# Kernel optimization log

Measured on AMD Instinct MI355X. Metric: run time of the kernel, lower is better.

The kernel has to match this reference:

```python
import jax, jax.numpy as jnp
import numpy as np

B, H, SQ, SKV, D = 2, 16, 2048, 2048, 64
SCALE = 8  # sqrt(head_dim)


def setup_inputs() -> dict:
    key = jax.random.key(0)
    kq, kk, kv, km = jax.random.split(key, 4)
    q = jax.random.normal(kq, (B, H, SQ, D), dtype=jnp.float32)
    k = jax.random.normal(kk, (B, H, SKV, D), dtype=jnp.float32)
    v = jax.random.normal(kv, (B, H, SKV, D), dtype=jnp.float32)
    mask = jax.random.normal(km, (1, 1, SQ, SKV), dtype=jnp.float32)
    return {"q": q, "k": k, "v": v, "mask": mask, "scale": SCALE}


def reference(q, k, v, mask, scale):
    # scores: [B, H, SQ, SKV]
    scores = jnp.einsum("bhqd,bhkd->bhqk", q, k) / scale
    scores = scores + mask  # broadcast additive mask
    probs = jax.nn.softmax(scores, axis=-1)
    # hidden: [B, H, SQ, D]
    return jnp.einsum("bhqk,bhkd->bhqd", probs, v)
```

## Files before the change

kernel.cpp:

```cpp
#include <hip/hip_runtime.h>
#include <hip/hip_bf16.h>

#define NB 2
#define NH 16
#define NSQ 2048
#define NSKV 2048
#define ND 64
#define NT (NSKV / 64)
#define LOG2E 1.4426950408889634f
#define BHSTRIDE (NSKV * ND)

typedef __attribute__((ext_vector_type(8))) short bf16x8;
typedef __attribute__((ext_vector_type(4))) float f32x4;

__device__ __forceinline__ short f2bf(float x) {
  union { float f; unsigned u; } c; c.f = x;
  unsigned r = c.u + 0x7fffu + ((c.u >> 16) & 1u);
  return (short)(r >> 16);
}
__device__ __forceinline__ unsigned pack_bf2(float lo, float hi) {
  union { __hip_bfloat162 h; unsigned u; } c;
  c.h = __float22bfloat162_rn(float2{lo, hi});
  return c.u;
}
__device__ __forceinline__ float u2f(unsigned u) {
  union { unsigned u; float f; } c; c.u = u; return c.f;
}
__device__ __forceinline__ float exp2_fast(float x) {
#if __has_builtin(__builtin_amdgcn_exp2f)
  return __builtin_amdgcn_exp2f(x);
#else
  return exp2f(x);
#endif
}

__device__ __forceinline__ int kvmap(int x) {
  return (x & 3) | (((x >> 4) & 1) << 2) | (((x >> 2) & 1) << 3)
       | (((x >> 3) & 1) << 4) | (x & 32);
}

__global__ void prep_k(const float* __restrict__ K, short* __restrict__ Kp) {
  const int bh = blockIdx.y, tile = blockIdx.x, tid = (int)threadIdx.x;
#pragma unroll
  for (int h = 0; h < 2; ++h) {
    const int u    = tid + h * 256;
    const int nt   = u >> 7, kc = (u >> 6) & 1, lane = u & 63;
    const int prow = nt * 16 + (lane & 15);
    const float* src = K + ((size_t)bh * NSKV + tile * 64 + kvmap(prow)) * ND
                         + kc * 32 + (lane >> 4) * 8;
    float4 a = *(const float4*)src, b = *(const float4*)(src + 4);
    bf16x8 w;
    w[0]=f2bf(a.x); w[1]=f2bf(a.y); w[2]=f2bf(a.z); w[3]=f2bf(a.w);
    w[4]=f2bf(b.x); w[5]=f2bf(b.y); w[6]=f2bf(b.z); w[7]=f2bf(b.w);
    *(bf16x8*)(Kp + (size_t)bh * BHSTRIDE + (size_t)tile * 4096 + u * 8) = w;
  }
}

__global__ void prep_vt(const float* __restrict__ V, short* __restrict__ Vp) {
  __shared__ float T[64][65];
  const int kv0 = blockIdx.x * 64;
  const int bh  = blockIdx.y;
  const int t   = (int)threadIdx.x;
  const float* src = V + ((size_t)bh * NSKV + kv0) * ND;
#pragma unroll
  for (int i = 0; i < 4; ++i) {
    float4 v = *(const float4*)(src + (size_t)((t >> 4) + 16 * i) * ND + (t & 15) * 4);
    T[(t >> 4) + 16 * i][(t & 15) * 4 + 0] = v.x;
    T[(t >> 4) + 16 * i][(t & 15) * 4 + 1] = v.y;
    T[(t >> 4) + 16 * i][(t & 15) * 4 + 2] = v.z;
    T[(t >> 4) + 16 * i][(t & 15) * 4 + 3] = v.w;
  }
  __syncthreads();
  const int d = t >> 2, c = t & 3;
  bf16x8 w0, w1;
#pragma unroll
  for (int j = 0; j < 8; ++j) w0[j] = f2bf(T[c * 16 + j][d]);
#pragma unroll
  for (int j = 0; j < 8; ++j) w1[j] = f2bf(T[c * 16 + 8 + j][d]);
  const int frag  = (d >> 4) * 2 + (c >> 1);
  const int lane0 = (((2 * c) & 3) << 4) | (d & 15);
  const int lane1 = (((2 * c + 1) & 3) << 4) | (d & 15);
  short* dstb = Vp + (size_t)bh * BHSTRIDE + (size_t)blockIdx.x * 4096 + frag * 512;
  *(bf16x8*)(dstb + lane0 * 8) = w0;
  *(bf16x8*)(dstb + lane1 * 8) = w1;
}

__global__ void prep_mt(const float* __restrict__ M, unsigned short* __restrict__ Mt) {
  const int qt = blockIdx.x;
  const int kt = blockIdx.y;
  const int t  = (int)threadIdx.x;
  const int rl = t >> 4;
  const int c  = t & 15;
  const int row = qt * 16 + rl;
  float4 v = *(const float4*)(M + (size_t)row * NSKV + kt * 64 + c * 4);
  const int nt   = 2 * (c >> 3) + (c & 1);
  const int lq   = (c >> 1) & 3;
  const int lane = lq * 16 + rl;
  ushort4 o;
  o.x = (unsigned short)f2bf(LOG2E * v.x);
  o.y = (unsigned short)f2bf(LOG2E * v.y);
  o.z = (unsigned short)f2bf(LOG2E * v.z);
  o.w = (unsigned short)f2bf(LOG2E * v.w);
  *(ushort4*)(Mt + (((size_t)qt * 32 + kt) * 64 + lane) * 16 + nt * 4) = o;
}

__global__ __launch_bounds__(256, 2)
void attn_fwd(const float* __restrict__ Q, const short* __restrict__ Kp,
              const short* __restrict__ Vp, const unsigned short* __restrict__ Mt,
              const void* __restrict__ scale_p, float* __restrict__ O)
{
  const int lin = (int)blockIdx.x + ((int)blockIdx.y << 4);
  const int swz = ((lin & 7) << 6) | (lin >> 3);
  const int qb  = swz & 15;
  const int bh  = swz >> 4;

  const int tid = (int)threadIdx.x;
  const int wv  = tid >> 6;
  const int ln  = tid & 63;
  const int l16 = ln & 15;
  const int lq  = ln >> 4;

  float scale_v;
  {
    union { int i; float f; } u;
    u.i = ((const int*)scale_p)[0];
    float af = fabsf(u.f);
    scale_v = (af >= 1e-6f && af <= 1e6f) ? u.f : (float)u.i;
  }
  const float qmul = LOG2E / scale_v;

  const int q0 = qb * 128;
  const short* Kb = Kp + (size_t)bh * BHSTRIDE;
  const short* Vb = Vp + (size_t)bh * BHSTRIDE;

  bf16x8 qf[2][2];
#pragma unroll
  for (int qs = 0; qs < 2; ++qs) {
    const float* qrow = Q + ((size_t)bh * NSQ + q0 + wv * 32 + qs * 16 + l16) * ND;
#pragma unroll
    for (int kc = 0; kc < 2; ++kc) {
      const float4* p = (const float4*)(qrow + kc * 32 + lq * 8);
      float4 a = p[0], b = p[1];
      bf16x8 f;
      f[0]=f2bf(a.x*qmul); f[1]=f2bf(a.y*qmul); f[2]=f2bf(a.z*qmul); f[3]=f2bf(a.w*qmul);
      f[4]=f2bf(b.x*qmul); f[5]=f2bf(b.y*qmul); f[6]=f2bf(b.z*qmul); f[7]=f2bf(b.w*qmul);
      qf[qs][kc] = f;
    }
  }

  f32x4 oa[2][4];
  f32x4 lacc[2];
#pragma unroll
  for (int qs = 0; qs < 2; ++qs) {
#pragma unroll
    for (int dt = 0; dt < 4; ++dt) { f32x4 z = {0.f,0.f,0.f,0.f}; oa[qs][dt] = z; }
    f32x4 z = {0.f,0.f,0.f,0.f}; lacc[qs] = z;
  }

  bf16x8 ones;
#pragma unroll
  for (int j = 0; j < 8; ++j) ones[j] = (short)0x3F80;

  const unsigned short* Mq0 = Mt + ((size_t)(qb * 8 + wv * 2)) * 32 * 64 * 16 + (size_t)ln * 16;
  const unsigned short* Mq1 = Mq0 + (size_t)32 * 64 * 16;

  union MU { uint4 q[2]; unsigned u[8]; };
  MU mc[2], mn[2];

  bf16x8 kfc[4][2], kfn[4][2], vf[4][2];
#pragma unroll
  for (int nt = 0; nt < 4; ++nt)
#pragma unroll
    for (int kc = 0; kc < 2; ++kc)
      kfc[nt][kc] = *(const bf16x8*)(Kb + (nt * 2 + kc) * 512 + ln * 8);
  mc[0].q[0] = *(const uint4*)(Mq0);
  mc[0].q[1] = *(const uint4*)(Mq0 + 8);
  mc[1].q[0] = *(const uint4*)(Mq1);
  mc[1].q[1] = *(const uint4*)(Mq1 + 8);

#pragma unroll 2
  for (int t = 0; t < NT; ++t) {
    const short* Vt0 = Vb + (size_t)t * 4096;
#pragma unroll
    for (int dt = 0; dt < 4; ++dt)
#pragma unroll
      for (int kc = 0; kc < 2; ++kc)
        vf[dt][kc] = *(const bf16x8*)(Vt0 + (dt * 2 + kc) * 512 + ln * 8);

    if (t + 1 < NT) {
      const short* Kt1 = Kb + (size_t)(t + 1) * 4096;
#pragma unroll
      for (int nt = 0; nt < 4; ++nt)
#pragma unroll
        for (int kc = 0; kc < 2; ++kc)
          kfn[nt][kc] = *(const bf16x8*)(Kt1 + (nt * 2 + kc) * 512 + ln * 8);
    }

    f32x4 s0[4];
    __builtin_amdgcn_s_setprio(1);
#pragma unroll
    for (int nt = 0; nt < 4; ++nt) {
      f32x4 a = {0.f,0.f,0.f,0.f};
      a = __builtin_amdgcn_mfma_f32_16x16x32_bf16(kfc[nt][0], qf[0][0], a, 0, 0, 0);
      a = __builtin_amdgcn_mfma_f32_16x16x32_bf16(kfc[nt][1], qf[0][1], a, 0, 0, 0);
      s0[nt] = a;
    }
    __builtin_amdgcn_s_setprio(0);

    bf16x8 pa0[2];
    {
#pragma unroll
      for (int nt = 0; nt < 4; ++nt) {
        const unsigned w0 = mc[0].u[nt * 2], w1 = mc[0].u[nt * 2 + 1];
        s0[nt][0] = exp2_fast(s0[nt][0] + u2f(w0 << 16));
        s0[nt][1] = exp2_fast(s0[nt][1] + u2f(w0 & 0xffff0000u));
        s0[nt][2] = exp2_fast(s0[nt][2] + u2f(w1 << 16));
        s0[nt][3] = exp2_fast(s0[nt][3] + u2f(w1 & 0xffff0000u));
      }
#pragma unroll
      for (int kc = 0; kc < 2; ++kc) {
        union { unsigned u[4]; bf16x8 v; } w;
        w.u[0] = pack_bf2(s0[2*kc][0],   s0[2*kc][1]);
        w.u[1] = pack_bf2(s0[2*kc][2],   s0[2*kc][3]);
        w.u[2] = pack_bf2(s0[2*kc+1][0], s0[2*kc+1][1]);
        w.u[3] = pack_bf2(s0[2*kc+1][2], s0[2*kc+1][3]);
        pa0[kc] = w.v;
      }
    }

    f32x4 s1[4];
    __builtin_amdgcn_s_setprio(1);
#pragma unroll
    for (int nt = 0; nt < 4; ++nt) {
      f32x4 a = {0.f,0.f,0.f,0.f};
      a = __builtin_amdgcn_mfma_f32_16x16x32_bf16(kfc[nt][0], qf[1][0], a, 0, 0, 0);
      a = __builtin_amdgcn_mfma_f32_16x16x32_bf16(kfc[nt][1], qf[1][1], a, 0, 0, 0);
      s1[nt] = a;
    }
    __builtin_amdgcn_s_setprio(0);

    if (t + 1 < NT) {
      const unsigned short* mp0 = Mq0 + (size_t)(t + 1) * 64 * 16;
      const unsigned short* mp1 = Mq1 + (size_t)(t + 1) * 64 * 16;
      mn[0].q[0] = *(const uint4*)(mp0);
      mn[0].q[1] = *(const uint4*)(mp0 + 8);
      mn[1].q[0] = *(const uint4*)(mp1);
      mn[1].q[1] = *(const uint4*)(mp1 + 8);
    }

    __builtin_amdgcn_s_setprio(1);
#pragma unroll
    for (int kc = 0; kc < 2; ++kc) {
#pragma unroll
      for (int dt = 0; dt < 4; ++dt)
        oa[0][dt] = __builtin_amdgcn_mfma_f32_16x16x32_bf16(pa0[kc], vf[dt][kc], oa[0][dt], 0, 0, 0);
      lacc[0] = __builtin_amdgcn_mfma_f32_16x16x32_bf16(pa0[kc], ones, lacc[0], 0, 0, 0);
    }
    __builtin_amdgcn_s_setprio(0);

    bf16x8 pa1[2];
    {
#pragma unroll
      for (int nt = 0; nt < 4; ++nt) {
        const unsigned w0 = mc[1].u[nt * 2], w1 = mc[1].u[nt * 2 + 1];
        s1[nt][0] = exp2_fast(s1[nt][0] + u2f(w0 << 16));
        s1[nt][1] = exp2_fast(s1[nt][1] + u2f(w0 & 0xffff0000u));
        s1[nt][2] = exp2_fast(s1[nt][2] + u2f(w1 << 16));
        s1[nt][3] = exp2_fast(s1[nt][3] + u2f(w1 & 0xffff0000u));
      }
#pragma unroll
      for (int kc = 0; kc < 2; ++kc) {
        union { unsigned u[4]; bf16x8 v; } w;
        w.u[0] = pack_bf2(s1[2*kc][0],   s1[2*kc][1]);
        w.u[1] = pack_bf2(s1[2*kc][2],   s1[2*kc][3]);
        w.u[2] = pack_bf2(s1[2*kc+1][0], s1[2*kc+1][1]);
        w.u[3] = pack_bf2(s1[2*kc+1][2], s1[2*kc+1][3]);
        pa1[kc] = w.v;
      }
    }

    __builtin_amdgcn_s_setprio(1);
#pragma unroll
    for (int kc = 0; kc < 2; ++kc) {
#pragma unroll
      for (int dt = 0; dt < 4; ++dt)
        oa[1][dt] = __builtin_amdgcn_mfma_f32_16x16x32_bf16(pa1[kc], vf[dt][kc], oa[1][dt], 0, 0, 0);
      lacc[1] = __builtin_amdgcn_mfma_f32_16x16x32_bf16(pa1[kc], ones, lacc[1], 0, 0, 0);
    }
    __builtin_amdgcn_s_setprio(0);

#pragma unroll
    for (int nt = 0; nt < 4; ++nt)
#pragma unroll
      for (int kc = 0; kc < 2; ++kc)
        kfc[nt][kc] = kfn[nt][kc];
    mc[0] = mn[0];
    mc[1] = mn[1];
  }

#pragma unroll
  for (int qs = 0; qs < 2; ++qs)
#pragma unroll
    for (int r = 0; r < 4; ++r) {
      const float inv = 1.0f / lacc[qs][r];
      float* orow = O + ((size_t)bh * NSQ + q0 + wv * 32 + qs * 16 + lq * 4 + r) * ND;
#pragma unroll
      for (int dt = 0; dt < 4; ++dt)
        orow[dt * 16 + l16] = oa[qs][dt][r] * inv;
    }
}

extern "C" void kernel_launch(void* const* d_in, const int* in_sizes, int n_in,
                              void* d_out, int out_size, void* d_ws, size_t ws_size,
                              hipStream_t stream) {
  const float* q     = (const float*)d_in[0];
  const float* k     = (const float*)d_in[1];
  const float* v     = (const float*)d_in[2];
  const float* mask  = (const float*)d_in[3];
  const void*  scale = (const void*)d_in[4];
  float* out = (float*)d_out;

  const size_t NELEM = (size_t)NB * NH * NSKV * ND;
  short* Kpk = (short*)d_ws;
  short* Vpk = Kpk + NELEM;
  unsigned short* Mtl = (unsigned short*)(Vpk + NELEM);

  prep_k<<<dim3(NSKV / 64, NB * NH), 256, 0, stream>>>(k, Kpk);
  prep_vt<<<dim3(NSKV / 64, NB * NH), 256, 0, stream>>>(v, Vpk);
  prep_mt<<<dim3(NSQ / 16, NSKV / 64), 256, 0, stream>>>(mask, Mtl);

  dim3 grid(NSQ / 128, NB * NH);
  attn_fwd<<<grid, 256, 0, stream>>>(q, Kpk, Vpk, Mtl, scale, out);
}
```

Measured before the change: 78.87 us.

## Stage K/V tiles through LDS via async loads and fold mask into MFMA accumulator

Replaces per-wave direct global register loads of K and V with a double-buffered LDS stage filled by global_load_lds. Each wave now loads one quarter of the tile and the tile is shared across the block through a barrier. The mask is fed in as the initial MFMA accumulator instead of being added before exp2, and it is kept in fp32 when the workspace is large enough. This cuts redundant global and L2 traffic for K/V and removes the per-element mask adds. In exchange it adds a __syncthreads per tile, uses more LDS, and doubles the mask bytes read in the fp32 path.

```diff
diff --git a/kernel.cpp b/kernel.cpp
--- a/kernel.cpp
+++ b/kernel.cpp
@@ -12,6 +12,8 @@
 
 typedef __attribute__((ext_vector_type(8))) short bf16x8;
 typedef __attribute__((ext_vector_type(4))) float f32x4;
+typedef __attribute__((address_space(1))) const unsigned gas_u32;
+typedef __attribute__((address_space(3))) unsigned las_u32;
 
 __device__ __forceinline__ short f2bf(float x) {
   union { float f; unsigned u; } c; c.f = x;
@@ -85,12 +87,21 @@
   *(bf16x8*)(dstb + lane1 * 8) = w1;
 }
 
+__global__ void prep_mf(const float* __restrict__ M, float* __restrict__ Mf) {
+  const int qt = blockIdx.x, kt = blockIdx.y, t = (int)threadIdx.x;
+  const int rl = t >> 4, c = t & 15;
+  const int row = qt * 16 + rl;
+  float4 v = *(const float4*)(M + (size_t)row * NSKV + kt * 64 + c * 4);
+  const int nt   = 2 * (c >> 3) + (c & 1);
+  const int lq   = (c >> 1) & 3;
+  const int lane = lq * 16 + rl;
+  float4 o = {LOG2E * v.x, LOG2E * v.y, LOG2E * v.z, LOG2E * v.w};
+  *(float4*)(Mf + (((size_t)qt * 32 + kt) * 64 + lane) * 16 + nt * 4) = o;
+}
+
 __global__ void prep_mt(const float* __restrict__ M, unsigned short* __restrict__ Mt) {
-  const int qt = blockIdx.x;
-  const int kt = blockIdx.y;
-  const int t  = (int)threadIdx.x;
-  const int rl = t >> 4;
-  const int c  = t & 15;
+  const int qt = blockIdx.x, kt = blockIdx.y, t = (int)threadIdx.x;
+  const int rl = t >> 4, c = t & 15;
   const int row = qt * 16 + rl;
   float4 v = *(const float4*)(M + (size_t)row * NSKV + kt * 64 + c * 4);
   const int nt   = 2 * (c >> 3) + (c & 1);
@@ -104,9 +115,10 @@
   *(ushort4*)(Mt + (((size_t)qt * 32 + kt) * 64 + lane) * 16 + nt * 4) = o;
 }
 
+template<bool MF32>
 __global__ __launch_bounds__(256, 2)
 void attn_fwd(const float* __restrict__ Q, const short* __restrict__ Kp,
-              const short* __restrict__ Vp, const unsigned short* __restrict__ Mt,
+              const short* __restrict__ Vp, const void* __restrict__ Mv,
               const void* __restrict__ scale_p, float* __restrict__ O)
 {
   const int lin = (int)blockIdx.x + ((int)blockIdx.y << 4);
@@ -132,6 +144,9 @@
   const int q0 = qb * 128;
   const short* Kb = Kp + (size_t)bh * BHSTRIDE;
   const short* Vb = Vp + (size_t)bh * BHSTRIDE;
+
+  __shared__ short Kl[2][4096];
+  __shared__ short Vl[2][4096];
 
   bf16x8 qf[2][2];
 #pragma unroll
@@ -161,141 +176,115 @@
 #pragma unroll
   for (int j = 0; j < 8; ++j) ones[j] = (short)0x3F80;
 
-  const unsigned short* Mq0 = Mt + ((size_t)(qb * 8 + wv * 2)) * 32 * 64 * 16 + (size_t)ln * 16;
-  const unsigned short* Mq1 = Mq0 + (size_t)32 * 64 * 16;
-
-  union MU { uint4 q[2]; unsigned u[8]; };
-  MU mc[2], mn[2];
-
-  bf16x8 kfc[4][2], kfn[4][2], vf[4][2];
-#pragma unroll
-  for (int nt = 0; nt < 4; ++nt)
-#pragma unroll
-    for (int kc = 0; kc < 2; ++kc)
-      kfc[nt][kc] = *(const bf16x8*)(Kb + (nt * 2 + kc) * 512 + ln * 8);
-  mc[0].q[0] = *(const uint4*)(Mq0);
-  mc[0].q[1] = *(const uint4*)(Mq0 + 8);
-  mc[1].q[0] = *(const uint4*)(Mq1);
-  mc[1].q[1] = *(const uint4*)(Mq1 + 8);
-
-#pragma unroll 2
-  for (int t = 0; t < NT; ++t) {
-    const short* Vt0 = Vb + (size_t)t * 4096;
-#pragma unroll
-    for (int dt = 0; dt < 4; ++dt)
-#pragma unroll
-      for (int kc = 0; kc < 2; ++kc)
-        vf[dt][kc] = *(const bf16x8*)(Vt0 + (dt * 2 + kc) * 512 + ln * 8);
-
+  const int ebytes = MF32 ? 4 : 2;
+  const char* M0 = (const char*)Mv + ((size_t)(qb * 8 + wv * 2) * 32768 + (size_t)ln * 16) * ebytes;
+  const char* M1 = M0 + (size_t)32768 * ebytes;
+
+  auto mload = [&](int t, float4* mf0, float4* mf1) {
+    if constexpr (MF32) {
+      const float* p0 = (const float*)(M0 + (size_t)t * 1024 * 4);
+      const float* p1 = (const float*)(M1 + (size_t)t * 1024 * 4);
+#pragma unroll
+      for (int nt = 0; nt < 4; ++nt) {
+        mf0[nt] = *(const float4*)(p0 + nt * 4);
+        mf1[nt] = *(const float4*)(p1 + nt * 4);
+      }
+    } else {
+      const unsigned short* p0 = (const unsigned short*)(M0 + (size_t)t * 1024 * 2);
+      const unsigned short* p1 = (const unsigned short*)(M1 + (size_t)t * 1024 * 2);
+      uint4 a0 = *(const uint4*)p0, b0 = *(const uint4*)(p0 + 8);
+      uint4 a1 = *(const uint4*)p1, b1 = *(const uint4*)(p1 + 8);
+      const unsigned u0[8] = {a0.x,a0.y,a0.z,a0.w,b0.x,b0.y,b0.z,b0.w};
+      const unsigned u1[8] = {a1.x,a1.y,a1.z,a1.w,b1.x,b1.y,b1.z,b1.w};
+#pragma unroll
+      for (int nt = 0; nt < 4; ++nt) {
+        mf0[nt] = float4{u2f(u0[nt*2] << 16), u2f(u0[nt*2] & 0xffff0000u),
+                         u2f(u0[nt*2+1] << 16), u2f(u0[nt*2+1] & 0xffff0000u)};
+        mf1[nt] = float4{u2f(u1[nt*2] << 16), u2f(u1[nt*2] & 0xffff0000u),
+                         u2f(u1[nt*2+1] << 16), u2f(u1[nt*2+1] & 0xffff0000u)};
+      }
+    }
+  };
+
+  auto stage = [&](int t, int buf) {
+    const short* ks = Kb + (size_t)t * 4096;
+    const short* vs = Vb + (size_t)t * 4096;
+#pragma unroll
+    for (int i = 0; i < 2; ++i) {
+      const int chunk = wv * 2 + i;
+      __builtin_amdgcn_global_load_lds((gas_u32*)(ks + chunk * 512 + ln * 8),
+                                       (las_u32*)&Kl[buf][chunk * 512], 16, 0, 0);
+      __builtin_amdgcn_global_load_lds((gas_u32*)(vs + chunk * 512 + ln * 8),
+                                       (las_u32*)&Vl[buf][chunk * 512], 16, 0, 0);
+    }
+  };
+
+  auto subtile = [&](bf16x8 (&kf)[4][2], bf16x8 (&vf)[4][2], int qs, float4* mf) {
+    f32x4 s[4];
+    __builtin_amdgcn_s_setprio(1);
+#pragma unroll
+    for (int nt = 0; nt < 4; ++nt) {
+      f32x4 a = *(const f32x4*)&mf[nt];
+      a = __builtin_amdgcn_mfma_f32_16x16x32_bf16(kf[nt][0], qf[qs][0], a, 0, 0, 0);
+      a = __builtin_amdgcn_mfma_f32_16x16x32_bf16(kf[nt][1], qf[qs][1], a, 0, 0, 0);
+      s[nt] = a;
+    }
+    __builtin_amdgcn_s_setprio(0);
+#pragma unroll
+    for (int nt = 0; nt < 4; ++nt) {
+      s[nt][0] = exp2_fast(s[nt][0]);
+      s[nt][1] = exp2_fast(s[nt][1]);
+      s[nt][2] = exp2_fast(s[nt][2]);
+      s[nt][3] = exp2_fast(s[nt][3]);
+    }
+    bf16x8 pa[2];
+#pragma unroll
+    for (int kc = 0; kc < 2; ++kc) {
+      union { unsigned u[4]; bf16x8 v; } w;
+      w.u[0] = pack_bf2(s[2*kc][0],   s[2*kc][1]);
+      w.u[1] = pack_bf2(s[2*kc][2],   s[2*kc][3]);
+      w.u[2] = pack_bf2(s[2*kc+1][0], s[2*kc+1][1]);
+      w.u[3] = pack_bf2(s[2*kc+1][2], s[2*kc+1][3]);
+      pa[kc] = w.v;
+    }
+    __builtin_amdgcn_s_setprio(1);
+#pragma unroll
+    for (int kc = 0; kc < 2; ++kc) {
+#pragma unroll
+      for (int dt = 0; dt < 4; ++dt)
+        oa[qs][dt] = __builtin_amdgcn_mfma_f32_16x16x32_bf16(pa[kc], vf[dt][kc], oa[qs][dt], 0, 0, 0);
+      lacc[qs] = __builtin_amdgcn_mfma_f32_16x16x32_bf16(pa[kc], ones, lacc[qs], 0, 0, 0);
+    }
+    __builtin_amdgcn_s_setprio(0);
+  };
+
+  auto tile = [&](int t, int buf, float4 (&mc0)[4], float4 (&mc1)[4],
+                  float4 (&mn0)[4], float4 (&mn1)[4]) {
     if (t + 1 < NT) {
-      const short* Kt1 = Kb + (size_t)(t + 1) * 4096;
-#pragma unroll
-      for (int nt = 0; nt < 4; ++nt)
-#pragma unroll
-        for (int kc = 0; kc < 2; ++kc)
-          kfn[nt][kc] = *(const bf16x8*)(Kt1 + (nt * 2 + kc) * 512 + ln * 8);
-    }
-
-    f32x4 s0[4];
-    __builtin_amdgcn_s_setprio(1);
-#pragma unroll
-    for (int nt = 0; nt < 4; ++nt) {
-      f32x4 a = {0.f,0.f,0.f,0.f};
-      a = __builtin_amdgcn_mfma_f32_16x16x32_bf16(kfc[nt][0], qf[0][0], a, 0, 0, 0);
-      a = __builtin_amdgcn_mfma_f32_16x16x32_bf16(kfc[nt][1], qf[0][1], a, 0, 0, 0);
-      s0[nt] = a;
-    }
-    __builtin_amdgcn_s_setprio(0);
-
-    bf16x8 pa0[2];
-    {
-#pragma unroll
-      for (int nt = 0; nt < 4; ++nt) {
-        const unsigned w0 = mc[0].u[nt * 2], w1 = mc[0].u[nt * 2 + 1];
-        s0[nt][0] = exp2_fast(s0[nt][0] + u2f(w0 << 16));
-        s0[nt][1] = exp2_fast(s0[nt][1] + u2f(w0 & 0xffff0000u));
-        s0[nt][2] = exp2_fast(s0[nt][2] + u2f(w1 << 16));
-        s0[nt][3] = exp2_fast(s0[nt][3] + u2f(w1 & 0xffff0000u));
+      stage(t + 1, buf ^ 1);
+      mload(t + 1, mn0, mn1);
+    }
+    bf16x8 kf[4][2], vf[4][2];
+#pragma unroll
+    for (int nt = 0; nt < 4; ++nt)
+#pragma unroll
+      for (int kc = 0; kc < 2; ++kc) {
+        kf[nt][kc] = *(const bf16x8*)&Kl[buf][(nt * 2 + kc) * 512 + ln * 8];
+        vf[nt][kc] = *(const bf16x8*)&Vl[buf][(nt * 2 + kc) * 512 + ln * 8];
       }
-#pragma unroll
-      for (int kc = 0; kc < 2; ++kc) {
-        union { unsigned u[4]; bf16x8 v; } w;
-        w.u[0] = pack_bf2(s0[2*kc][0],   s0[2*kc][1]);
-        w.u[1] = pack_bf2(s0[2*kc][2],   s0[2*kc][3]);
-        w.u[2] = pack_bf2(s0[2*kc+1][0], s0[2*kc+1][1]);
-        w.u[3] = pack_bf2(s0[2*kc+1][2], s0[2*kc+1][3]);
-        pa0[kc] = w.v;
-      }
-    }
-
-    f32x4 s1[4];
-    __builtin_amdgcn_s_setprio(1);
-#pragma unroll
-    for (int nt = 0; nt < 4; ++nt) {
-      f32x4 a = {0.f,0.f,0.f,0.f};
-      a = __builtin_amdgcn_mfma_f32_16x16x32_bf16(kfc[nt][0], qf[1][0], a, 0, 0, 0);
-      a = __builtin_amdgcn_mfma_f32_16x16x32_bf16(kfc[nt][1], qf[1][1], a, 0, 0, 0);
-      s1[nt] = a;
-    }
-    __builtin_amdgcn_s_setprio(0);
-
-    if (t + 1 < NT) {
-      const unsigned short* mp0 = Mq0 + (size_t)(t + 1) * 64 * 16;
-      const unsigned short* mp1 = Mq1 + (size_t)(t + 1) * 64 * 16;
-      mn[0].q[0] = *(const uint4*)(mp0);
-      mn[0].q[1] = *(const uint4*)(mp0 + 8);
-      mn[1].q[0] = *(const uint4*)(mp1);
-      mn[1].q[1] = *(const uint4*)(mp1 + 8);
-    }
-
-    __builtin_amdgcn_s_setprio(1);
-#pragma unroll
-    for (int kc = 0; kc < 2; ++kc) {
-#pragma unroll
-      for (int dt = 0; dt < 4; ++dt)
-        oa[0][dt] = __builtin_amdgcn_mfma_f32_16x16x32_bf16(pa0[kc], vf[dt][kc], oa[0][dt], 0, 0, 0);
-      lacc[0] = __builtin_amdgcn_mfma_f32_16x16x32_bf16(pa0[kc], ones, lacc[0], 0, 0, 0);
-    }
-    __builtin_amdgcn_s_setprio(0);
-
-    bf16x8 pa1[2];
-    {
-#pragma unroll
-      for (int nt = 0; nt < 4; ++nt) {
-        const unsigned w0 = mc[1].u[nt * 2], w1 = mc[1].u[nt * 2 + 1];
-        s1[nt][0] = exp2_fast(s1[nt][0] + u2f(w0 << 16));
-        s1[nt][1] = exp2_fast(s1[nt][1] + u2f(w0 & 0xffff0000u));
-        s1[nt][2] = exp2_fast(s1[nt][2] + u2f(w1 << 16));
-        s1[nt][3] = exp2_fast(s1[nt][3] + u2f(w1 & 0xffff0000u));
-      }
-#pragma unroll
-      for (int kc = 0; kc < 2; ++kc) {
-        union { unsigned u[4]; bf16x8 v; } w;
-        w.u[0] = pack_bf2(s1[2*kc][0],   s1[2*kc][1]);
-        w.u[1] = pack_bf2(s1[2*kc][2],   s1[2*kc][3]);
-        w.u[2] = pack_bf2(s1[2*kc+1][0], s1[2*kc+1][1]);
-        w.u[3] = pack_bf2(s1[2*kc+1][2], s1[2*kc+1][3]);
-        pa1[kc] = w.v;
-      }
-    }
-
-    __builtin_amdgcn_s_setprio(1);
-#pragma unroll
-    for (int kc = 0; kc < 2; ++kc) {
-#pragma unroll
-      for (int dt = 0; dt < 4; ++dt)
-        oa[1][dt] = __builtin_amdgcn_mfma_f32_16x16x32_bf16(pa1[kc], vf[dt][kc], oa[1][dt], 0, 0, 0);
-      lacc[1] = __builtin_amdgcn_mfma_f32_16x16x32_bf16(pa1[kc], ones, lacc[1], 0, 0, 0);
-    }
-    __builtin_amdgcn_s_setprio(0);
-
-#pragma unroll
-    for (int nt = 0; nt < 4; ++nt)
-#pragma unroll
-      for (int kc = 0; kc < 2; ++kc)
-        kfc[nt][kc] = kfn[nt][kc];
-    mc[0] = mn[0];
-    mc[1] = mn[1];
+    subtile(kf, vf, 0, mc0);
+    subtile(kf, vf, 1, mc1);
+    __syncthreads();
+  };
+
+  float4 mA0[4], mA1[4], mB0[4], mB1[4];
+  stage(0, 0);
+  mload(0, mA0, mA1);
+  __syncthreads();
+
+  for (int t = 0; t < NT; t += 2) {
+    tile(t,     0, mA0, mA1, mB0, mB1);
+    tile(t + 1, 1, mB0, mB1, mA0, mA1);
   }
 
 #pragma unroll
@@ -323,12 +312,20 @@
   const size_t NELEM = (size_t)NB * NH * NSKV * ND;
   short* Kpk = (short*)d_ws;
   short* Vpk = Kpk + NELEM;
-  unsigned short* Mtl = (unsigned short*)(Vpk + NELEM);
+  void*  Mreg = (void*)(Vpk + NELEM);
+
+  const size_t need_f32 = NELEM * 2 * 2 + (size_t)NSQ * NSKV * 4;
+  const bool mf32 = (ws_size >= need_f32);
 
   prep_k<<<dim3(NSKV / 64, NB * NH), 256, 0, stream>>>(k, Kpk);
   prep_vt<<<dim3(NSKV / 64, NB * NH), 256, 0, stream>>>(v, Vpk);
-  prep_mt<<<dim3(NSQ / 16, NSKV / 64), 256, 0, stream>>>(mask, Mtl);
 
   dim3 grid(NSQ / 128, NB * NH);
-  attn_fwd<<<grid, 256, 0, stream>>>(q, Kpk, Vpk, Mtl, scale, out);
-}
+  if (mf32) {
+    prep_mf<<<dim3(NSQ / 16, NSKV / 64), 256, 0, stream>>>(mask, (float*)Mreg);
+    attn_fwd<true><<<grid, 256, 0, stream>>>(q, Kpk, Vpk, Mreg, scale, out);
+  } else {
+    prep_mt<<<dim3(NSQ / 16, NSKV / 64), 256, 0, stream>>>(mask, (unsigned short*)Mreg);
+    attn_fwd<false><<<grid, 256, 0, stream>>>(q, Kpk, Vpk, Mreg, scale, out);
+  }
+}
```

New measurement: 93.30 us. +18.3%, slower.
